# Kernel optimization log

Hardware: AMD Instinct MI355X
Metric: run time of the kernel (lower is better)

The kernel has to match this reference:

```python
import jax, jax.numpy as jnp
import numpy as np

N = 100000


def seg_mean(feat, src, dst, n):
    # gather at src, scatter-mean at dst (PyG mean aggr: 0 for isolated nodes)
    s = jax.ops.segment_sum(feat[src], dst, num_segments=n)
    cnt = jax.ops.segment_sum(jnp.ones((src.shape[0],), feat.dtype), dst, num_segments=n)
    return s / jnp.maximum(cnt, 1.0)[:, None]


def setup_inputs() -> dict:
    key = jax.random.key(0)
    ks = jax.random.split(key, 8)
    d_in, d_h = 64, 32
    E = 1_250_000
    inp = {
        "x": jax.random.normal(ks[0], (N, d_in), jnp.float32),
        "W1_pos": jax.random.normal(ks[1], (2 * d_in, d_h), jnp.float32) * 0.05,
        "b1_pos": jnp.zeros((d_h,), jnp.float32),
        "W1_neg": jax.random.normal(ks[2], (2 * d_in, d_h), jnp.float32) * 0.05,
        "b1_neg": jnp.zeros((d_h,), jnp.float32),
        "W2_pos": jax.random.normal(ks[3], (3 * d_h, d_h), jnp.float32) * 0.05,
        "b2_pos": jnp.zeros((d_h,), jnp.float32),
        "W2_neg": jax.random.normal(ks[4], (3 * d_h, d_h), jnp.float32) * 0.05,
        "b2_neg": jnp.zeros((d_h,), jnp.float32),
        "pos_edge_index": jax.random.randint(ks[5], (2, E), 0, N, jnp.int64),
        "neg_edge_index": jax.random.randint(ks[6], (2, E), 0, N, jnp.int64),
    }
    return inp


def reference(x, W1_pos, b1_pos, W1_neg, b1_neg, W2_pos, b2_pos, W2_neg, b2_neg,
              pos_edge_index, neg_edge_index):
    ps, pd = pos_edge_index[0], pos_edge_index[1]
    ns, nd = neg_edge_index[0], neg_edge_index[1]
    n = x.shape[0]

    # --- layer 1 (first_aggr=True) ---
    ap = seg_mean(x, ps, pd, n)          # [N, 64]
    an = seg_mean(x, ns, nd, n)
    out_p = jnp.concatenate([ap, x], -1) @ W1_pos + b1_pos   # [N, 32]
    out_n = jnp.concatenate([an, x], -1) @ W1_neg + b1_neg
    z = jnp.tanh(jnp.concatenate([out_p, out_n], -1))        # [N, 64]

    # --- layer 2 (first_aggr=False) ---
    d_h = out_p.shape[-1]
    zp, zn = z[:, :d_h], z[:, d_h:]
    out_p = jnp.concatenate([seg_mean(zp, ps, pd, n), seg_mean(zn, ns, nd, n), zp], -1) @ W2_pos + b2_pos
    out_n = jnp.concatenate([seg_mean(zn, ps, pd, n), seg_mean(zp, ns, nd, n), zn], -1) @ W2_neg + b2_neg
    z = jnp.tanh(jnp.concatenate([out_p, out_n], -1))
    return z
```

## Files before the change

### kernel.cpp

```cpp
#include <hip/hip_runtime.h>
#include <math.h>


typedef _Float16 h4 __attribute__((ext_vector_type(4)));
typedef _Float16 h8 __attribute__((ext_vector_type(8)));
typedef float f32x4 __attribute__((ext_vector_type(4)));

__device__ inline h8 shflx8(h8 v, int m) {
    int4 i = __builtin_bit_cast(int4, v);
    i.x = __shfl_xor(i.x, m);
    i.y = __shfl_xor(i.y, m);
    i.z = __shfl_xor(i.z, m);
    i.w = __shfl_xor(i.w, m);
    return __builtin_bit_cast(h8, i);
}

__device__ inline float fast_tanh(float v) {
    float e = __expf(2.0f * v);
    return 1.0f - 2.0f / (e + 1.0f);
}


#define BSHIFT 9
#define BSIZE  512
#define NBMAX  512
#define CAP    8192

__global__ void __launch_bounds__(256) bucket_k(
    const int* __restrict__ pos, const int* __restrict__ neg,
    int* __restrict__ pcnt, unsigned* __restrict__ ebuf,
    int E, int n, int nb)
{
    __shared__ int cnt[NBMAX], gbase[NBMAX];
    const int K = 32;
    int tid = threadIdx.x;
    int base = blockIdx.x * (256 * K);

    for (int i = tid; i < nb; i += 256) cnt[i] = 0;
    __syncthreads();

    unsigned val[K], pr[K];
    #pragma unroll
    for (int k = 0; k < K; ++k) {
        int e = base + k * 256 + tid;
        pr[k] = 0xFFFFFFFFu;
        if (e < 2 * E) {
            int nd, sr;
            if (e < E) { nd = pos[E + e];                 sr = pos[e]; }
            else       { int ee = e - E; nd = n + neg[E + ee]; sr = neg[ee]; }
            int p = nd >> BSHIFT;
            val[k] = ((unsigned)(nd & (BSIZE - 1)) << 17) | (unsigned)sr;
            int rank = atomicAdd(&cnt[p], 1);
            pr[k] = ((unsigned)p << 13) | (unsigned)rank;
        }
    }
    __syncthreads();
    for (int i = tid; i < nb; i += 256) {
        int c = cnt[i];
        gbase[i] = c ? atomicAdd(&pcnt[i], c) : 0;
    }
    __syncthreads();
    #pragma unroll
    for (int k = 0; k < K; ++k) {
        if (pr[k] != 0xFFFFFFFFu) {
            int p = (int)(pr[k] >> 13);
            int off = gbase[p] + (int)(pr[k] & 0x1FFFu);
            if (off < CAP) ebuf[(size_t)p * CAP + off] = val[k];
        }
    }
}

__global__ void __launch_bounds__(512) bscan_k(
    const int* __restrict__ pcnt, int* __restrict__ bbase, int nb)
{
    __shared__ int s[512];
    int tid = threadIdx.x;
    int v = (tid < nb) ? pcnt[tid] : 0;
    s[tid] = v;
    __syncthreads();
    for (int off = 1; off < 512; off <<= 1) {
        int t = (tid >= off) ? s[tid - off] : 0;
        __syncthreads();
        s[tid] += t;
        __syncthreads();
    }
    if (tid < nb) bbase[tid] = s[tid] - v;
}

__global__ void __launch_bounds__(256) scatter_k(
    const unsigned* __restrict__ ebuf, const int* __restrict__ pcnt,
    const int* __restrict__ bbase,
    int* __restrict__ cur, int* __restrict__ col, int n)
{
    __shared__ int lcnt[BSIZE], lbase[BSIZE], sc[256];
    __shared__ int lcol[CAP];
    int p = blockIdx.x;
    int tid = threadIdx.x;
    int n2 = 2 * n;
    int lo = p << BSHIFT;
    int nn = min(BSIZE, n2 - lo);
    int cnt = min(pcnt[p], CAP);
    const unsigned* buf = ebuf + (size_t)p * CAP;

    lcnt[tid] = 0; lcnt[tid + 256] = 0;
    __syncthreads();
    for (int i = tid; i < cnt; i += 256) {
        unsigned v = buf[i];
        atomicAdd(&lcnt[v >> 17], 1);
    }
    __syncthreads();
    int a0 = lcnt[2 * tid], a1 = lcnt[2 * tid + 1];
    int s = a0 + a1;
    sc[tid] = s;
    __syncthreads();
    for (int off = 1; off < 256; off <<= 1) {
        int t = (tid >= off) ? sc[tid - off] : 0;
        __syncthreads();
        sc[tid] += t;
        __syncthreads();
    }
    int excl = sc[tid] - s;
    lbase[2 * tid] = excl;
    lbase[2 * tid + 1] = excl + a0;
    __syncthreads();
    int gb = bbase[p];
    for (int i = tid; i < nn; i += 256)
        cur[lo + i] = gb + lbase[i] + lcnt[i];
    __syncthreads();
    for (int i = tid; i < cnt; i += 256) {
        unsigned v = buf[i];
        int rel = (int)(v >> 17);
        int slot = atomicAdd(&lbase[rel], 1);
        lcol[slot] = (int)(v & 0x1FFFFu);
    }
    __syncthreads();
    for (int t = tid; t < cnt; t += 256)
        col[gb + t] = lcol[t];
}


__global__ void __launch_bounds__(256) cvt_k(
    const float4* __restrict__ x, h4* __restrict__ xh, int n4)
{
    int i = blockIdx.x * 256 + threadIdx.x;
    if (i < n4) {
        float4 v = x[i];
        h4 o = { (_Float16)v.x, (_Float16)v.y, (_Float16)v.z, (_Float16)v.w };
        xh[i] = o;
    }
}


__device__ inline float b1map(const float* W1p, const float* W1n, int k, int c)
{
    if (c < 32) {
        if (k < 64)   return W1p[k * 32 + c];
        if (k >= 128) return W1p[(k - 64) * 32 + c];
        return 0.0f;
    } else {
        int cn = c - 32;
        if (k >= 64)  return W1n[(k - 64) * 32 + cn];
        return 0.0f;
    }
}

__device__ inline float b2map(const float* W2p, const float* W2n, int k, int c)
{
    if (c < 32) {
        if (k < 32)               return W2p[k * 32 + c];
        if (k >= 96 && k < 128)   return W2p[(k - 96 + 32) * 32 + c];
        if (k >= 128 && k < 160)  return W2p[(k - 128 + 64) * 32 + c];
        return 0.0f;
    } else {
        int cn = c - 32;
        if (k >= 32 && k < 64)    return W2n[(k - 32) * 32 + cn];
        if (k >= 64 && k < 96)    return W2n[(k - 64 + 32) * 32 + cn];
        if (k >= 160)             return W2n[(k - 160 + 64) * 32 + cn];
        return 0.0f;
    }
}

__global__ void __launch_bounds__(256) prep_k(
    const float* __restrict__ W1p, const float* __restrict__ W1n,
    const float* __restrict__ W2p, const float* __restrict__ W2n,
    _Float16* __restrict__ Bpack)
{
    int slot = blockIdx.x * 256 + threadIdx.x;
    if (slot >= 2 * 24 * 64) return;
    int mat  = slot / (24 * 64);
    int rem  = slot % (24 * 64);
    int fg   = rem / 64;
    int lane = rem % 64;
    int kk = fg >> 2, nt = fg & 3;
    int g = lane >> 4, m = lane & 15;
    _Float16* dst = Bpack + (size_t)slot * 8;
    int c = nt * 16 + m;
    #pragma unroll
    for (int j = 0; j < 8; ++j) {
        int k = kk * 32 + g * 8 + j;
        float v = mat ? b2map(W2p, W2n, k, c) : b1map(W1p, W1n, k, c);
        dst[j] = (_Float16)v;
    }
}


__global__ void __launch_bounds__(256) agg_k(
    const h8* __restrict__ feat8,
    const int* __restrict__ cur, const int* __restrict__ col,
    h8* __restrict__ ag8, int n)
{
    int tid = threadIdx.x;
    int wave = tid >> 6, lane = tid & 63;
    int g = lane >> 3, f = lane & 7;
    int list = g >> 2;
    int sub = g & 3;

    int stride = gridDim.x * 4;
    for (int node = blockIdx.x * 4 + wave; node < n; node += stride) {
        int idx = list ? n + node : node;
        int r0 = idx ? cur[idx - 1] : 0;
        int r1 = cur[idx];

        h8 acc = {};
        #pragma unroll 2
        for (int it = r0 + sub; it < r1; it += 4)
            acc = acc + feat8[(unsigned)(col[it] * 8 + f)];
        acc = acc + shflx8(acc, 8);
        acc = acc + shflx8(acc, 16);
        _Float16 inv = (_Float16)(1.0f / (float)max(r1 - r0, 1));
        h8 iv = { inv, inv, inv, inv, inv, inv, inv, inv };
        acc = acc * iv;
        if (sub == 0)
            ag8[(unsigned)(node * 16 + list * 8 + f)] = acc;
    }
}


#define ROWP 200

__global__ void __launch_bounds__(256) gemm_k(
    const h8* __restrict__ ag8, const h8* __restrict__ feat8,
    const h8* __restrict__ Bp,
    const float* __restrict__ bp, const float* __restrict__ bn,
    float* __restrict__ outf, _Float16* __restrict__ outh,
    int f32out, int n)
{
    __shared__ _Float16 A_lds[64 * ROWP];
    int tid = threadIdx.x;
    int base = blockIdx.x * 64;

    for (int ch = tid; ch < 64 * 24; ch += 256) {
        int r = ch / 24, p = ch % 24;
        int row = min(base + r, n - 1);
        h8 v = (p < 16) ? ag8[(size_t)row * 16 + p]
                        : feat8[(size_t)row * 8 + (p - 16)];
        *(h8*)&A_lds[r * ROWP + p * 8] = v;
    }
    __syncthreads();

    int w = tid >> 6, lane = tid & 63;
    int m = lane & 15, g = lane >> 4;

    h8 a[6];
    #pragma unroll
    for (int kk = 0; kk < 6; ++kk)
        a[kk] = *(const h8*)&A_lds[(w * 16 + m) * ROWP + kk * 32 + g * 8];

    #pragma unroll
    for (int nt = 0; nt < 4; ++nt) {
        f32x4 acc = { 0.f, 0.f, 0.f, 0.f };
        #pragma unroll
        for (int kk = 0; kk < 6; ++kk) {
            h8 b = Bp[(kk * 4 + nt) * 64 + lane];
            acc = __builtin_amdgcn_mfma_f32_16x16x32_f16(a[kk], b, acc, 0, 0, 0);
        }
        int colc = nt * 16 + m;
        float bias = (colc < 32) ? bp[colc] : bn[colc - 32];
        #pragma unroll
        for (int reg = 0; reg < 4; ++reg) {
            int node = base + w * 16 + g * 4 + reg;
            if (node < n) {
                float val = fast_tanh(acc[reg] + bias);
                if (f32out) outf[(size_t)node * 64 + colc] = val;
                else        outh[(size_t)node * 64 + colc] = (_Float16)val;
            }
        }
    }
}

extern "C" void kernel_launch(void* const* d_in, const int* in_sizes, int n_in,
                              void* d_out, int out_size, void* d_ws, size_t ws_size,
                              hipStream_t stream)
{
    const float* x   = (const float*)d_in[0];
    const float* W1p = (const float*)d_in[1];
    const float* b1p = (const float*)d_in[2];
    const float* W1n = (const float*)d_in[3];
    const float* b1n = (const float*)d_in[4];
    const float* W2p = (const float*)d_in[5];
    const float* b2p = (const float*)d_in[6];
    const float* W2n = (const float*)d_in[7];
    const float* b2n = (const float*)d_in[8];
    const int*   pos = (const int*)d_in[9];
    const int*   neg = (const int*)d_in[10];

    int n = in_sizes[0] / 64;
    int E = in_sizes[9] / 2;
    int n2 = 2 * n;
    int nb = (n2 + BSIZE - 1) / BSIZE;

    int*      pcnt  = (int*)d_ws;
    int*      bbase = pcnt + NBMAX;
    int*      cur   = bbase + NBMAX;
    int*      col   = cur + n2;
    _Float16* Bpack = (_Float16*)(col + 2 * (size_t)E);
    _Float16* xh    = Bpack + 2 * 24 * 64 * 8;
    unsigned* ebuf  = (unsigned*)(xh + (size_t)n * 64);
    _Float16* zh    = (_Float16*)ebuf;
    h8*       ag8   = (h8*)d_out;

    hipMemsetAsync(pcnt, 0, NBMAX * sizeof(int), stream);

    int bblocks = (2 * E + 8191) / 8192;
    bucket_k<<<bblocks, 256, 0, stream>>>(pos, neg, pcnt, ebuf, E, n, nb);
    bscan_k <<<1, 512, 0, stream>>>(pcnt, bbase, nb);
    scatter_k<<<nb, 256, 0, stream>>>(ebuf, pcnt, bbase, cur, col, n);

    int n4 = n * 16;
    cvt_k <<<(n4 + 255) / 256, 256, 0, stream>>>((const float4*)x, (h4*)xh, n4);
    prep_k<<<12, 256, 0, stream>>>(W1p, W1n, W2p, W2n, Bpack);

    int ablocks = 2048;
    int gblocks = (n + 63) / 64;

    agg_k <<<ablocks, 256, 0, stream>>>((const h8*)xh, cur, col, ag8, n);
    gemm_k<<<gblocks, 256, 0, stream>>>(ag8, (const h8*)xh, (const h8*)Bpack,
                                        b1p, b1n, nullptr, zh, 0, n);

    agg_k <<<ablocks, 256, 0, stream>>>((const h8*)zh, cur, col, ag8, n);
    gemm_k<<<gblocks, 256, 0, stream>>>(ag8, (const h8*)zh,
                                        (const h8*)(Bpack + 24 * 64 * 8),
                                        b2p, b2n, (float*)d_out, nullptr, 1, n);
}
```

Measured before the change: 285.7 us.

## Fuse neighbor aggregation into GEMM, fold block scan into scatter, merge prep kernels

```diff
diff --git a/kernel.cpp b/kernel.cpp
--- a/kernel.cpp
+++ b/kernel.cpp
@@ -70,29 +70,11 @@
     }
 }
 
-__global__ void __launch_bounds__(512) bscan_k(
-    const int* __restrict__ pcnt, int* __restrict__ bbase, int nb)
-{
-    __shared__ int s[512];
-    int tid = threadIdx.x;
-    int v = (tid < nb) ? pcnt[tid] : 0;
-    s[tid] = v;
-    __syncthreads();
-    for (int off = 1; off < 512; off <<= 1) {
-        int t = (tid >= off) ? s[tid - off] : 0;
-        __syncthreads();
-        s[tid] += t;
-        __syncthreads();
-    }
-    if (tid < nb) bbase[tid] = s[tid] - v;
-}
-
 __global__ void __launch_bounds__(256) scatter_k(
     const unsigned* __restrict__ ebuf, const int* __restrict__ pcnt,
-    const int* __restrict__ bbase,
-    int* __restrict__ cur, int* __restrict__ col, int n)
-{
-    __shared__ int lcnt[BSIZE], lbase[BSIZE], sc[256];
+    int* __restrict__ cur, int* __restrict__ col, int n, int nb)
+{
+    __shared__ int lcnt[BSIZE], lbase[BSIZE], sc[256], bb[NBMAX];
     __shared__ int lcol[CAP];
     int p = blockIdx.x;
     int tid = threadIdx.x;
@@ -102,6 +84,23 @@
     int cnt = min(pcnt[p], CAP);
     const unsigned* buf = ebuf + (size_t)p * CAP;
 
+    {
+        int a0 = (2 * tid     < nb) ? pcnt[2 * tid]     : 0;
+        int a1 = (2 * tid + 1 < nb) ? pcnt[2 * tid + 1] : 0;
+        int s = a0 + a1;
+        sc[tid] = s;
+        __syncthreads();
+        for (int off = 1; off < 256; off <<= 1) {
+            int t = (tid >= off) ? sc[tid - off] : 0;
+            __syncthreads();
+            sc[tid] += t;
+            __syncthreads();
+        }
+        int excl = sc[tid] - s;
+        bb[2 * tid] = excl;
+        bb[2 * tid + 1] = excl + a0;
+    }
+
     lcnt[tid] = 0; lcnt[tid + 256] = 0;
     __syncthreads();
     for (int i = tid; i < cnt; i += 256) {
@@ -123,7 +122,7 @@
     lbase[2 * tid] = excl;
     lbase[2 * tid + 1] = excl + a0;
     __syncthreads();
-    int gb = bbase[p];
+    int gb = bb[p];
     for (int i = tid; i < nn; i += 256)
         cur[lo + i] = gb + lbase[i] + lcnt[i];
     __syncthreads();
@@ -136,18 +135,6 @@
     __syncthreads();
     for (int t = tid; t < cnt; t += 256)
         col[gb + t] = lcol[t];
-}
-
-
-__global__ void __launch_bounds__(256) cvt_k(
-    const float4* __restrict__ x, h4* __restrict__ xh, int n4)
-{
-    int i = blockIdx.x * 256 + threadIdx.x;
-    if (i < n4) {
-        float4 v = x[i];
-        h4 o = { (_Float16)v.x, (_Float16)v.y, (_Float16)v.z, (_Float16)v.w };
-        xh[i] = o;
-    }
 }
 
 
@@ -180,12 +167,22 @@
     }
 }
 
-__global__ void __launch_bounds__(256) prep_k(
+__global__ void __launch_bounds__(256) cvtprep_k(
+    const float4* __restrict__ x, h4* __restrict__ xh, int n4, int cvtBlocks,
     const float* __restrict__ W1p, const float* __restrict__ W1n,
     const float* __restrict__ W2p, const float* __restrict__ W2n,
     _Float16* __restrict__ Bpack)
 {
-    int slot = blockIdx.x * 256 + threadIdx.x;
+    if ((int)blockIdx.x < cvtBlocks) {
+        int i = blockIdx.x * 256 + threadIdx.x;
+        if (i < n4) {
+            float4 v = x[i];
+            h4 o = { (_Float16)v.x, (_Float16)v.y, (_Float16)v.z, (_Float16)v.w };
+            xh[i] = o;
+        }
+        return;
+    }
+    int slot = (blockIdx.x - cvtBlocks) * 256 + threadIdx.x;
     if (slot >= 2 * 24 * 64) return;
     int mat  = slot / (24 * 64);
     int rem  = slot % (24 * 64);
@@ -204,42 +201,11 @@
 }
 
 
-__global__ void __launch_bounds__(256) agg_k(
+#define ROWP 200
+
+__global__ void __launch_bounds__(256) layer_k(
     const h8* __restrict__ feat8,
     const int* __restrict__ cur, const int* __restrict__ col,
-    h8* __restrict__ ag8, int n)
-{
-    int tid = threadIdx.x;
-    int wave = tid >> 6, lane = tid & 63;
-    int g = lane >> 3, f = lane & 7;
-    int list = g >> 2;
-    int sub = g & 3;
-
-    int stride = gridDim.x * 4;
-    for (int node = blockIdx.x * 4 + wave; node < n; node += stride) {
-        int idx = list ? n + node : node;
-        int r0 = idx ? cur[idx - 1] : 0;
-        int r1 = cur[idx];
-
-        h8 acc = {};
-        #pragma unroll 2
-        for (int it = r0 + sub; it < r1; it += 4)
-            acc = acc + feat8[(unsigned)(col[it] * 8 + f)];
-        acc = acc + shflx8(acc, 8);
-        acc = acc + shflx8(acc, 16);
-        _Float16 inv = (_Float16)(1.0f / (float)max(r1 - r0, 1));
-        h8 iv = { inv, inv, inv, inv, inv, inv, inv, inv };
-        acc = acc * iv;
-        if (sub == 0)
-            ag8[(unsigned)(node * 16 + list * 8 + f)] = acc;
-    }
-}
-
-
-#define ROWP 200
-
-__global__ void __launch_bounds__(256) gemm_k(
-    const h8* __restrict__ ag8, const h8* __restrict__ feat8,
     const h8* __restrict__ Bp,
     const float* __restrict__ bp, const float* __restrict__ bn,
     float* __restrict__ outf, _Float16* __restrict__ outh,
@@ -248,23 +214,45 @@
     __shared__ _Float16 A_lds[64 * ROWP];
     int tid = threadIdx.x;
     int base = blockIdx.x * 64;
-
-    for (int ch = tid; ch < 64 * 24; ch += 256) {
-        int r = ch / 24, p = ch % 24;
-        int row = min(base + r, n - 1);
-        h8 v = (p < 16) ? ag8[(size_t)row * 16 + p]
-                        : feat8[(size_t)row * 8 + (p - 16)];
-        *(h8*)&A_lds[r * ROWP + p * 8] = v;
-    }
-    __syncthreads();
-
     int w = tid >> 6, lane = tid & 63;
-    int m = lane & 15, g = lane >> 4;
-
+
+    {
+        int g = lane >> 3, f = lane & 7;
+        int list = g >> 2;
+        int sub = g & 3;
+        for (int t = 0; t < 16; ++t) {
+            int node = base + w * 16 + t;
+            if (node >= n) break;
+            int idx = list ? n + node : node;
+            int r0 = idx ? cur[idx - 1] : 0;
+            int r1 = cur[idx];
+            h8 acc = {};
+            #pragma unroll 2
+            for (int it = r0 + sub; it < r1; it += 4)
+                acc = acc + feat8[(unsigned)(col[it] * 8 + f)];
+            acc = acc + shflx8(acc, 8);
+            acc = acc + shflx8(acc, 16);
+            _Float16 inv = (_Float16)(1.0f / (float)max(r1 - r0, 1));
+            h8 iv = { inv, inv, inv, inv, inv, inv, inv, inv };
+            acc = acc * iv;
+            if (sub == 0)
+                *(h8*)&A_lds[(w * 16 + t) * ROWP + list * 64 + f * 8] = acc;
+        }
+    }
+    for (int ch = lane; ch < 16 * 8; ch += 64) {
+        int t = ch >> 3, pch = ch & 7;
+        int row = base + w * 16 + t;
+        if (row < n)
+            *(h8*)&A_lds[(w * 16 + t) * ROWP + 128 + pch * 8] =
+                feat8[(size_t)row * 8 + pch];
+    }
+    __syncthreads();
+
+    int m = lane & 15, g4 = lane >> 4;
     h8 a[6];
     #pragma unroll
     for (int kk = 0; kk < 6; ++kk)
-        a[kk] = *(const h8*)&A_lds[(w * 16 + m) * ROWP + kk * 32 + g * 8];
+        a[kk] = *(const h8*)&A_lds[(w * 16 + m) * ROWP + kk * 32 + g4 * 8];
 
     #pragma unroll
     for (int nt = 0; nt < 4; ++nt) {
@@ -278,7 +266,7 @@
         float bias = (colc < 32) ? bp[colc] : bn[colc - 32];
         #pragma unroll
         for (int reg = 0; reg < 4; ++reg) {
-            int node = base + w * 16 + g * 4 + reg;
+            int node = base + w * 16 + g4 * 4 + reg;
             if (node < n) {
                 float val = fast_tanh(acc[reg] + bias);
                 if (f32out) outf[(size_t)node * 64 + colc] = val;
@@ -310,35 +298,29 @@
     int nb = (n2 + BSIZE - 1) / BSIZE;
 
     int*      pcnt  = (int*)d_ws;
-    int*      bbase = pcnt + NBMAX;
-    int*      cur   = bbase + NBMAX;
+    int*      cur   = pcnt + NBMAX;
     int*      col   = cur + n2;
     _Float16* Bpack = (_Float16*)(col + 2 * (size_t)E);
     _Float16* xh    = Bpack + 2 * 24 * 64 * 8;
     unsigned* ebuf  = (unsigned*)(xh + (size_t)n * 64);
     _Float16* zh    = (_Float16*)ebuf;
-    h8*       ag8   = (h8*)d_out;
 
     hipMemsetAsync(pcnt, 0, NBMAX * sizeof(int), stream);
 
     int bblocks = (2 * E + 8191) / 8192;
     bucket_k<<<bblocks, 256, 0, stream>>>(pos, neg, pcnt, ebuf, E, n, nb);
-    bscan_k <<<1, 512, 0, stream>>>(pcnt, bbase, nb);
-    scatter_k<<<nb, 256, 0, stream>>>(ebuf, pcnt, bbase, cur, col, n);
+    scatter_k<<<nb, 256, 0, stream>>>(ebuf, pcnt, cur, col, n, nb);
 
     int n4 = n * 16;
-    cvt_k <<<(n4 + 255) / 256, 256, 0, stream>>>((const float4*)x, (h4*)xh, n4);
-    prep_k<<<12, 256, 0, stream>>>(W1p, W1n, W2p, W2n, Bpack);
-
-    int ablocks = 2048;
-    int gblocks = (n + 63) / 64;
-
-    agg_k <<<ablocks, 256, 0, stream>>>((const h8*)xh, cur, col, ag8, n);
-    gemm_k<<<gblocks, 256, 0, stream>>>(ag8, (const h8*)xh, (const h8*)Bpack,
-                                        b1p, b1n, nullptr, zh, 0, n);
-
-    agg_k <<<ablocks, 256, 0, stream>>>((const h8*)zh, cur, col, ag8, n);
-    gemm_k<<<gblocks, 256, 0, stream>>>(ag8, (const h8*)zh,
-                                        (const h8*)(Bpack + 24 * 64 * 8),
-                                        b2p, b2n, (float*)d_out, nullptr, 1, n);
-}
+    int cvtBlocks = (n4 + 255) / 256;
+    cvtprep_k<<<cvtBlocks + 12, 256, 0, stream>>>(
+        (const float4*)x, (h4*)xh, n4, cvtBlocks, W1p, W1n, W2p, W2n, Bpack);
+
+    int lblocks = (n + 63) / 64;
+    layer_k<<<lblocks, 256, 0, stream>>>((const h8*)xh, cur, col,
+                                         (const h8*)Bpack, b1p, b1n,
+                                         nullptr, zh, 0, n);
+    layer_k<<<lblocks, 256, 0, stream>>>((const h8*)zh, cur, col,
+                                         (const h8*)(Bpack + 24 * 64 * 8),
+                                         b2p, b2n, (float*)d_out, nullptr, 1, n);
+}
```

Result: slower. 328.0 us (+14.8%).

## Fuse bucket, convert and weight-pack kernels; fold bucket scan into scatter; widen agg lanes

Applied to the files above, without the earlier changes.

```diff
diff --git a/kernel.cpp b/kernel.cpp
--- a/kernel.cpp
+++ b/kernel.cpp
@@ -26,15 +26,83 @@
 #define NBMAX  512
 #define CAP    8192
 
-__global__ void __launch_bounds__(256) bucket_k(
+
+__device__ inline float b1map(const float* W1p, const float* W1n, int k, int c)
+{
+    if (c < 32) {
+        if (k < 64)   return W1p[k * 32 + c];
+        if (k >= 128) return W1p[(k - 64) * 32 + c];
+        return 0.0f;
+    } else {
+        int cn = c - 32;
+        if (k >= 64)  return W1n[(k - 64) * 32 + cn];
+        return 0.0f;
+    }
+}
+
+__device__ inline float b2map(const float* W2p, const float* W2n, int k, int c)
+{
+    if (c < 32) {
+        if (k < 32)               return W2p[k * 32 + c];
+        if (k >= 96 && k < 128)   return W2p[(k - 96 + 32) * 32 + c];
+        if (k >= 128 && k < 160)  return W2p[(k - 128 + 64) * 32 + c];
+        return 0.0f;
+    } else {
+        int cn = c - 32;
+        if (k >= 32 && k < 64)    return W2n[(k - 32) * 32 + cn];
+        if (k >= 64 && k < 96)    return W2n[(k - 64 + 32) * 32 + cn];
+        if (k >= 160)             return W2n[(k - 160 + 64) * 32 + cn];
+        return 0.0f;
+    }
+}
+
+
+__global__ void __launch_bounds__(256) mega_k(
     const int* __restrict__ pos, const int* __restrict__ neg,
     int* __restrict__ pcnt, unsigned* __restrict__ ebuf,
-    int E, int n, int nb)
-{
+    int E, int n, int nb, int bblocks,
+    const float4* __restrict__ x, h4* __restrict__ xh, int n4, int cvtBlocks,
+    const float* __restrict__ W1p, const float* __restrict__ W1n,
+    const float* __restrict__ W2p, const float* __restrict__ W2n,
+    _Float16* __restrict__ Bpack)
+{
+    int tid = threadIdx.x;
+    int bid = blockIdx.x;
+
+    if (bid >= bblocks) {
+        int cb = bid - bblocks;
+        if (cb < cvtBlocks) {
+            int i = cb * 256 + tid;
+            if (i < n4) {
+                float4 v = x[i];
+                h4 o = { (_Float16)v.x, (_Float16)v.y, (_Float16)v.z, (_Float16)v.w };
+                xh[i] = o;
+            }
+        } else {
+            int slot = (cb - cvtBlocks) * 256 + tid;
+            if (slot < 2 * 24 * 64) {
+                int mat  = slot / (24 * 64);
+                int rem  = slot % (24 * 64);
+                int fg   = rem / 64;
+                int lane = rem % 64;
+                int kk = fg >> 2, nt = fg & 3;
+                int g = lane >> 4, m = lane & 15;
+                _Float16* dst = Bpack + (size_t)slot * 8;
+                int c = nt * 16 + m;
+                #pragma unroll
+                for (int j = 0; j < 8; ++j) {
+                    int k = kk * 32 + g * 8 + j;
+                    float v = mat ? b2map(W2p, W2n, k, c) : b1map(W1p, W1n, k, c);
+                    dst[j] = (_Float16)v;
+                }
+            }
+        }
+        return;
+    }
+
     __shared__ int cnt[NBMAX], gbase[NBMAX];
     const int K = 32;
-    int tid = threadIdx.x;
-    int base = blockIdx.x * (256 * K);
+    int base = bid * (256 * K);
 
     for (int i = tid; i < nb; i += 256) cnt[i] = 0;
     __syncthreads();
@@ -70,29 +138,11 @@
     }
 }
 
-__global__ void __launch_bounds__(512) bscan_k(
-    const int* __restrict__ pcnt, int* __restrict__ bbase, int nb)
-{
-    __shared__ int s[512];
-    int tid = threadIdx.x;
-    int v = (tid < nb) ? pcnt[tid] : 0;
-    s[tid] = v;
-    __syncthreads();
-    for (int off = 1; off < 512; off <<= 1) {
-        int t = (tid >= off) ? s[tid - off] : 0;
-        __syncthreads();
-        s[tid] += t;
-        __syncthreads();
-    }
-    if (tid < nb) bbase[tid] = s[tid] - v;
-}
-
 __global__ void __launch_bounds__(256) scatter_k(
     const unsigned* __restrict__ ebuf, const int* __restrict__ pcnt,
-    const int* __restrict__ bbase,
-    int* __restrict__ cur, int* __restrict__ col, int n)
-{
-    __shared__ int lcnt[BSIZE], lbase[BSIZE], sc[256];
+    int* __restrict__ cur, int* __restrict__ col, int n, int nb)
+{
+    __shared__ int lcnt[BSIZE], lbase[BSIZE], sc[256], bb[NBMAX];
     __shared__ int lcol[CAP];
     int p = blockIdx.x;
     int tid = threadIdx.x;
@@ -102,6 +152,23 @@
     int cnt = min(pcnt[p], CAP);
     const unsigned* buf = ebuf + (size_t)p * CAP;
 
+    {
+        int a0 = (2 * tid     < nb) ? pcnt[2 * tid]     : 0;
+        int a1 = (2 * tid + 1 < nb) ? pcnt[2 * tid + 1] : 0;
+        int s = a0 + a1;
+        sc[tid] = s;
+        __syncthreads();
+        for (int off = 1; off < 256; off <<= 1) {
+            int t = (tid >= off) ? sc[tid - off] : 0;
+            __syncthreads();
+            sc[tid] += t;
+            __syncthreads();
+        }
+        int excl = sc[tid] - s;
+        bb[2 * tid] = excl;
+        bb[2 * tid + 1] = excl + a0;
+    }
+
     lcnt[tid] = 0; lcnt[tid + 256] = 0;
     __syncthreads();
     for (int i = tid; i < cnt; i += 256) {
@@ -123,7 +190,7 @@
     lbase[2 * tid] = excl;
     lbase[2 * tid + 1] = excl + a0;
     __syncthreads();
-    int gb = bbase[p];
+    int gb = bb[p];
     for (int i = tid; i < nn; i += 256)
         cur[lo + i] = gb + lbase[i] + lcnt[i];
     __syncthreads();
@@ -139,71 +206,6 @@
 }
 
 
-__global__ void __launch_bounds__(256) cvt_k(
-    const float4* __restrict__ x, h4* __restrict__ xh, int n4)
-{
-    int i = blockIdx.x * 256 + threadIdx.x;
-    if (i < n4) {
-        float4 v = x[i];
-        h4 o = { (_Float16)v.x, (_Float16)v.y, (_Float16)v.z, (_Float16)v.w };
-        xh[i] = o;
-    }
-}
-
-
-__device__ inline float b1map(const float* W1p, const float* W1n, int k, int c)
-{
-    if (c < 32) {
-        if (k < 64)   return W1p[k * 32 + c];
-        if (k >= 128) return W1p[(k - 64) * 32 + c];
-        return 0.0f;
-    } else {
-        int cn = c - 32;
-        if (k >= 64)  return W1n[(k - 64) * 32 + cn];
-        return 0.0f;
-    }
-}
-
-__device__ inline float b2map(const float* W2p, const float* W2n, int k, int c)
-{
-    if (c < 32) {
-        if (k < 32)               return W2p[k * 32 + c];
-        if (k >= 96 && k < 128)   return W2p[(k - 96 + 32) * 32 + c];
-        if (k >= 128 && k < 160)  return W2p[(k - 128 + 64) * 32 + c];
-        return 0.0f;
-    } else {
-        int cn = c - 32;
-        if (k >= 32 && k < 64)    return W2n[(k - 32) * 32 + cn];
-        if (k >= 64 && k < 96)    return W2n[(k - 64 + 32) * 32 + cn];
-        if (k >= 160)             return W2n[(k - 160 + 64) * 32 + cn];
-        return 0.0f;
-    }
-}
-
-__global__ void __launch_bounds__(256) prep_k(
-    const float* __restrict__ W1p, const float* __restrict__ W1n,
-    const float* __restrict__ W2p, const float* __restrict__ W2n,
-    _Float16* __restrict__ Bpack)
-{
-    int slot = blockIdx.x * 256 + threadIdx.x;
-    if (slot >= 2 * 24 * 64) return;
-    int mat  = slot / (24 * 64);
-    int rem  = slot % (24 * 64);
-    int fg   = rem / 64;
-    int lane = rem % 64;
-    int kk = fg >> 2, nt = fg & 3;
-    int g = lane >> 4, m = lane & 15;
-    _Float16* dst = Bpack + (size_t)slot * 8;
-    int c = nt * 16 + m;
-    #pragma unroll
-    for (int j = 0; j < 8; ++j) {
-        int k = kk * 32 + g * 8 + j;
-        float v = mat ? b2map(W2p, W2n, k, c) : b1map(W1p, W1n, k, c);
-        dst[j] = (_Float16)v;
-    }
-}
-
-
 __global__ void __launch_bounds__(256) agg_k(
     const h8* __restrict__ feat8,
     const int* __restrict__ cur, const int* __restrict__ col,
@@ -211,9 +213,9 @@
 {
     int tid = threadIdx.x;
     int wave = tid >> 6, lane = tid & 63;
-    int g = lane >> 3, f = lane & 7;
-    int list = g >> 2;
-    int sub = g & 3;
+    int s = lane >> 2, f = lane & 3;
+    int list = s >> 3;
+    int sub = s & 7;
 
     int stride = gridDim.x * 4;
     for (int node = blockIdx.x * 4 + wave; node < n; node += stride) {
@@ -221,17 +223,25 @@
         int r0 = idx ? cur[idx - 1] : 0;
         int r1 = cur[idx];
 
-        h8 acc = {};
+        h8 acc0 = {}, acc1 = {};
         #pragma unroll 2
-        for (int it = r0 + sub; it < r1; it += 4)
-            acc = acc + feat8[(unsigned)(col[it] * 8 + f)];
-        acc = acc + shflx8(acc, 8);
-        acc = acc + shflx8(acc, 16);
+        for (int it = r0 + sub; it < r1; it += 8) {
+            unsigned srcb = (unsigned)col[it] * 8;
+            acc0 = acc0 + feat8[srcb + f];
+            acc1 = acc1 + feat8[srcb + 4 + f];
+        }
+        acc0 = acc0 + shflx8(acc0, 4);
+        acc1 = acc1 + shflx8(acc1, 4);
+        acc0 = acc0 + shflx8(acc0, 8);
+        acc1 = acc1 + shflx8(acc1, 8);
+        acc0 = acc0 + shflx8(acc0, 16);
+        acc1 = acc1 + shflx8(acc1, 16);
         _Float16 inv = (_Float16)(1.0f / (float)max(r1 - r0, 1));
         h8 iv = { inv, inv, inv, inv, inv, inv, inv, inv };
-        acc = acc * iv;
-        if (sub == 0)
-            ag8[(unsigned)(node * 16 + list * 8 + f)] = acc;
+        if (sub == 0) {
+            ag8[(unsigned)(node * 16 + list * 8 + f)]     = acc0 * iv;
+            ag8[(unsigned)(node * 16 + list * 8 + 4 + f)] = acc1 * iv;
+        }
     }
 }
 
@@ -310,8 +320,7 @@
     int nb = (n2 + BSIZE - 1) / BSIZE;
 
     int*      pcnt  = (int*)d_ws;
-    int*      bbase = pcnt + NBMAX;
-    int*      cur   = bbase + NBMAX;
+    int*      cur   = pcnt + NBMAX;
     int*      col   = cur + n2;
     _Float16* Bpack = (_Float16*)(col + 2 * (size_t)E);
     _Float16* xh    = Bpack + 2 * 24 * 64 * 8;
@@ -322,13 +331,15 @@
     hipMemsetAsync(pcnt, 0, NBMAX * sizeof(int), stream);
 
     int bblocks = (2 * E + 8191) / 8192;
-    bucket_k<<<bblocks, 256, 0, stream>>>(pos, neg, pcnt, ebuf, E, n, nb);
-    bscan_k <<<1, 512, 0, stream>>>(pcnt, bbase, nb);
-    scatter_k<<<nb, 256, 0, stream>>>(ebuf, pcnt, bbase, cur, col, n);
-
     int n4 = n * 16;
-    cvt_k <<<(n4 + 255) / 256, 256, 0, stream>>>((const float4*)x, (h4*)xh, n4);
-    prep_k<<<12, 256, 0, stream>>>(W1p, W1n, W2p, W2n, Bpack);
+    int cvtBlocks = (n4 + 255) / 256;
+
+    mega_k<<<bblocks + cvtBlocks + 12, 256, 0, stream>>>(
+        pos, neg, pcnt, ebuf, E, n, nb, bblocks,
+        (const float4*)x, (h4*)xh, n4, cvtBlocks,
+        W1p, W1n, W2p, W2n, Bpack);
+
+    scatter_k<<<nb, 256, 0, stream>>>(ebuf, pcnt, cur, col, n, nb);
 
     int ablocks = 2048;
     int gblocks = (n + 63) / 64;
```

Result: faster. 274.5 us (-3.9%).
